# Optimization experiments

Measured on AMD Instinct MI355X. Metric: run time of the kernel, lower is better.

## Reference

```python
import jax, jax.numpy as jnp
import numpy as np

B, T_IN, T_OUT = 256, 256, 32
E, H, Y, V = 512, 1024, 1024, 32000


def gru_cell(x, h, Wih, Whh, bih, bhh):
    # torch GRU gate order: r, z, n
    gi = x @ Wih.T + bih
    gh = h @ Whh.T + bhh
    ir, iz, inn = jnp.split(gi, 3, axis=-1)
    hr, hz, hn = jnp.split(gh, 3, axis=-1)
    r = jax.nn.sigmoid(ir + hr)
    z = jax.nn.sigmoid(iz + hz)
    n = jnp.tanh(inn + r * hn)
    return (1.0 - z) * n + z * h


def setup_inputs() -> dict:
    key = jax.random.key(0)
    ks = jax.random.split(key, 32)
    s = 0.05
    p = lambda k, shape: (jax.random.normal(k, shape, jnp.float32) * s)
    inp = {
        'x': jax.random.randint(ks[0], (B, T_IN), 0, V),
        'y': (jax.random.uniform(ks[1], (B, T_OUT, Y)) < 0.01).astype(jnp.float32),
        'emb': p(ks[2], (V, E)),
        # encoder layer 0 (input E) and layer 1 (input H)
        'enc_Wih0': p(ks[3], (3 * H, E)), 'enc_Whh0': p(ks[4], (3 * H, H)),
        'enc_bih0': p(ks[5], (3 * H,)), 'enc_bhh0': p(ks[6], (3 * H,)),
        'enc_Wih1': p(ks[7], (3 * H, H)), 'enc_Whh1': p(ks[8], (3 * H, H)),
        'enc_bih1': p(ks[9], (3 * H,)), 'enc_bhh1': p(ks[10], (3 * H,)),
        # decoder layer 0 (input Y) and layer 1 (input H)
        'dec_Wih0': p(ks[11], (3 * H, Y)), 'dec_Whh0': p(ks[12], (3 * H, H)),
        'dec_bih0': p(ks[13], (3 * H,)), 'dec_bhh0': p(ks[14], (3 * H,)),
        'dec_Wih1': p(ks[15], (3 * H, H)), 'dec_Whh1': p(ks[16], (3 * H, H)),
        'dec_bih1': p(ks[17], (3 * H,)), 'dec_bhh1': p(ks[18], (3 * H,)),
        # mapping: Linear(2H -> Y) followed by log-softmax
        'map_W': p(ks[19], (Y, 2 * H)), 'map_b': p(ks[20], (Y,)),
    }
    return inp


def reference(x, y, emb,
              enc_Wih0, enc_Whh0, enc_bih0, enc_bhh0,
              enc_Wih1, enc_Whh1, enc_bih1, enc_bhh1,
              dec_Wih0, dec_Whh0, dec_bih0, dec_bhh0,
              dec_Wih1, dec_Whh1, dec_bih1, dec_bhh1,
              map_W, map_b):
    batch = x.shape[0]
    h_dim = enc_Whh0.shape[1]

    # ---- encoder: 2-layer GRU over seq_in, h0 = 0 ----
    seq = emb[x].transpose(1, 0, 2)  # [T_in, B, E]
    finals = []
    for prm in ((enc_Wih0, enc_Whh0, enc_bih0, enc_bhh0),
                (enc_Wih1, enc_Whh1, enc_bih1, enc_bhh1)):
        def step(h, xt, prm=prm):
            hn = gru_cell(xt, h, *prm)
            return hn, hn
        hT, seq = jax.lax.scan(step, jnp.zeros((batch, h_dim), seq.dtype), seq)
        finals.append(hT)
    enc_out = seq.transpose(1, 0, 2)  # [B, T_in, H]

    # ---- decoder: teacher-forced, one step at a time ----
    y_shift = jnp.concatenate([jnp.zeros((batch, 1, y.shape[2]), y.dtype), y[:, :-1]], axis=1)
    ys_in = y_shift.transpose(1, 0, 2)  # [T_out, B, Y]
    ys_t = y.transpose(1, 0, 2)         # [T_out, B, Y]
    dec0 = (dec_Wih0, dec_Whh0, dec_bih0, dec_bhh0)
    dec1 = (dec_Wih1, dec_Whh1, dec_bih1, dec_bhh1)

    def dec_step(carry, inp):
        h1, h2 = carry
        y_in, y_t = inp
        h1 = gru_cell(y_in, h1, *dec0)
        h2 = gru_cell(h1, h2, *dec1)           # dec_out == top-layer hidden
        scores = jnp.einsum('bsh,bh->bs', enc_out, h2)
        alpha = jax.nn.softmax(scores, axis=-1)          # over encoder positions
        attn = jnp.einsum('bsh,bs->bh', enc_out, alpha)  # [B, H]
        logits = jnp.concatenate([attn, h2], axis=1) @ map_W.T + map_b
        logp = jax.nn.log_softmax(logits, axis=-1)
        loss_t = -(logp * y_t).sum()
        return (h1, h2), loss_t

    _, losses = jax.lax.scan(dec_step, (finals[0], finals[1]), (ys_in, ys_t))
    return losses.sum() / y.sum()
```

## Files before the change

### kernel.cpp

```cpp
#include <hip/hip_runtime.h>
#include <hip/hip_bf16.h>
#include <math.h>

#define BATCH 256
#define T_IN 256
#define T_OUT 32
#define E_DIM 512
#define H_DIM 1024
#define Y_DIM 1024
#define G_DIM 3072

typedef __attribute__((ext_vector_type(8))) __bf16 bf16x8;
typedef __attribute__((ext_vector_type(4))) float f32x4;
typedef __attribute__((ext_vector_type(4))) unsigned int u32x4;

__device__ __forceinline__ unsigned short f2bf_raw(float x) {
    unsigned int u = __builtin_bit_cast(unsigned int, x);
    u += 0x7FFFu + ((u >> 16) & 1u);
    return (unsigned short)(u >> 16);
}
__device__ __forceinline__ float bf2f(short s) {
    unsigned int u = ((unsigned int)(unsigned short)s) << 16;
    return __builtin_bit_cast(float, u);
}
__device__ __forceinline__ f32x4 mfma16(bf16x8 a, bf16x8 b, f32x4 c) {
    return __builtin_amdgcn_mfma_f32_16x16x32_bf16(a, b, c, 0, 0, 0);
}
__device__ __forceinline__ bf16x8 ldsb8(const short* p) {
    return __builtin_bit_cast(bf16x8, *(const u32x4*)p);
}

__global__ __launch_bounds__(256) void f32_to_bf16(
    const float* __restrict__ src, short* __restrict__ dst, int n4)
{
    for (int i = blockIdx.x * 256 + threadIdx.x; i < n4; i += gridDim.x * 256) {
        float4 f = *(const float4*)(src + 4 * (size_t)i);
        short4 o;
        o.x = (short)f2bf_raw(f.x);
        o.y = (short)f2bf_raw(f.y);
        o.z = (short)f2bf_raw(f.z);
        o.w = (short)f2bf_raw(f.w);
        *(short4*)(dst + 4 * (size_t)i) = o;
    }
}

struct CellArgs {
    const float* Af; const short* Ab; const int* gat; int gs; int lda; int Kx;
    const short* Wih; const short* Whh;
    const float* bih; const float* bhh;
    const short* hbf;
    const float* hf;
    float* houtf; short* houtbf; short* copy;
    int active;
};

__global__ __launch_bounds__(256) void cell_kernel(CellArgs cA, CellArgs cB)
{
    const CellArgs a = blockIdx.z ? cB : cA;
    if (!a.active) return;

    __shared__ __align__(16) short As[2 * 1280];
    __shared__ __align__(16) short Ws[6 * 2560];

    const int tid = threadIdx.x;
    const int bm = blockIdx.x * 32;
    const int bn = blockIdx.y * 64;

    const int sr = (tid >> 2) & 31;
    const int ss = tid >> 7;
    const int wr = tid >> 2;
    const int ch = (tid & 3) * 8;

    const float* axf = nullptr;
    const short* axb = nullptr;
    if (a.Af) {
        int ridx = a.gat ? a.gat[(size_t)(bm + sr) * a.gs] : (bm + sr);
        axf = a.Af + (size_t)ridx * a.lda + ch;
    } else if (a.Ab) {
        axb = a.Ab + (size_t)(bm + sr) * a.lda + ch;
    }
    const short* ahb = a.hbf + (size_t)(bm + sr) * H_DIM + ch;

    const short* wsrc[6];
    #pragma unroll
    for (int g = 0; g < 3; ++g) {
        wsrc[g]     = a.Wih + (size_t)(g * H_DIM + bn + wr) * a.Kx + ch;
        wsrc[g + 3] = a.Whh + (size_t)(g * H_DIM + bn + wr) * H_DIM + ch;
    }
    short* adst  = &As[ss * 1280 + sr * 40 + ch];
    short* wdst0 = &Ws[wr * 40 + ch];

    const int lane = tid & 63;
    const int w = tid >> 6;
    const int lr = lane & 15;
    const int ko = (lane >> 4) * 8;
    const short* pax0 = &As[lr * 40 + ko];
    const short* pax1 = &As[(16 + lr) * 40 + ko];
    const short* pah0 = &As[1280 + lr * 40 + ko];
    const short* pah1 = &As[1280 + (16 + lr) * 40 + ko];
    const int wc = (w * 16 + lr) * 40 + ko;

    f32x4 accI[3][2] = {{{0.f,0.f,0.f,0.f}}};
    f32x4 accH[3][2] = {{{0.f,0.f,0.f,0.f}}};

    const int Kx = a.Kx;
    for (int k0 = 0; k0 < H_DIM; k0 += 32) {
        const bool xact = (k0 < Kx);
        u32x4 av = {0u, 0u, 0u, 0u};
        if (ss) {
            av = *(const u32x4*)(ahb + k0);
        } else if (xact) {
            if (axb) {
                av = *(const u32x4*)(axb + k0);
            } else if (axf) {
                float4 f0 = *(const float4*)(axf + k0);
                float4 f1 = *(const float4*)(axf + k0 + 4);
                av.x = ((unsigned)f2bf_raw(f0.y) << 16) | f2bf_raw(f0.x);
                av.y = ((unsigned)f2bf_raw(f0.w) << 16) | f2bf_raw(f0.z);
                av.z = ((unsigned)f2bf_raw(f1.y) << 16) | f2bf_raw(f1.x);
                av.w = ((unsigned)f2bf_raw(f1.w) << 16) | f2bf_raw(f1.z);
            }
        }
        if (ss || xact) *(u32x4*)adst = av;
        #pragma unroll
        for (int i = 0; i < 6; ++i) {
            if (i >= 3 || xact)
                *(u32x4*)(wdst0 + i * 2560) = *(const u32x4*)(wsrc[i] + k0);
        }
        __syncthreads();
        bf16x8 ah0 = ldsb8(pah0), ah1 = ldsb8(pah1);
        #pragma unroll
        for (int g = 0; g < 3; ++g) {
            bf16x8 wh = ldsb8(&Ws[(g + 3) * 2560 + wc]);
            accH[g][0] = mfma16(ah0, wh, accH[g][0]);
            accH[g][1] = mfma16(ah1, wh, accH[g][1]);
        }
        if (xact) {
            bf16x8 ax0 = ldsb8(pax0), ax1 = ldsb8(pax1);
            #pragma unroll
            for (int g = 0; g < 3; ++g) {
                bf16x8 wi = ldsb8(&Ws[g * 2560 + wc]);
                accI[g][0] = mfma16(ax0, wi, accI[g][0]);
                accI[g][1] = mfma16(ax1, wi, accI[g][1]);
            }
        }
        __syncthreads();
    }

    const int j = bn + w * 16 + lr;
    const float bi0 = a.bih[j], bi1 = a.bih[H_DIM + j], bi2 = a.bih[2 * H_DIM + j];
    const float bh0 = a.bhh[j], bh1 = a.bhh[H_DIM + j], bh2 = a.bhh[2 * H_DIM + j];
    #pragma unroll
    for (int rh = 0; rh < 2; ++rh) {
        #pragma unroll
        for (int q = 0; q < 4; ++q) {
            int row = bm + rh * 16 + (lane >> 4) * 4 + q;
            float ir = accI[0][rh][q] + bi0, hr = accH[0][rh][q] + bh0;
            float iz = accI[1][rh][q] + bi1, hz = accH[1][rh][q] + bh1;
            float in_ = accI[2][rh][q] + bi2, hn = accH[2][rh][q] + bh2;
            float r = 1.f / (1.f + expf(-(ir + hr)));
            float z = 1.f / (1.f + expf(-(iz + hz)));
            float n = tanhf(in_ + r * hn);
            size_t oi = (size_t)row * H_DIM + j;
            float hv = a.hf[oi];
            float o = (1.f - z) * n + z * hv;
            a.houtf[oi] = o;
            short ob = (short)f2bf_raw(o);
            a.houtbf[oi] = ob;
            if (a.copy) a.copy[oi] = ob;
        }
    }
}

__global__ __launch_bounds__(256) void score_gemm(
    const short* __restrict__ h2all, const short* __restrict__ enc,
    float* __restrict__ S)
{
    const int st = blockIdx.x;
    const int b = blockIdx.y;
    __shared__ __align__(16) short Hs[32 * 40];
    __shared__ __align__(16) short Es[64 * 40];
    const int tid = threadIdx.x;
    const int ch = (tid & 3) * 8;
    const int hrow = (tid >> 2) & 31;
    const int erow = tid >> 2;
    const short* hsrc = h2all + ((size_t)hrow * BATCH + b) * H_DIM + ch;
    const short* esrc = enc + ((size_t)(st * 64 + erow) * BATCH + b) * H_DIM + ch;
    short* hdst = &Hs[hrow * 40 + ch];
    short* edst = &Es[erow * 40 + ch];

    const int lane = tid & 63, w = tid >> 6;
    const int lr = lane & 15, ko = (lane >> 4) * 8;
    f32x4 acc0 = {0.f, 0.f, 0.f, 0.f}, acc1 = acc0;
    for (int k0 = 0; k0 < H_DIM; k0 += 32) {
        if (tid < 128) *(u32x4*)hdst = *(const u32x4*)(hsrc + k0);
        *(u32x4*)edst = *(const u32x4*)(esrc + k0);
        __syncthreads();
        bf16x8 e = ldsb8(&Es[(w * 16 + lr) * 40 + ko]);
        bf16x8 h0v = ldsb8(&Hs[lr * 40 + ko]);
        bf16x8 h1v = ldsb8(&Hs[(16 + lr) * 40 + ko]);
        acc0 = mfma16(h0v, e, acc0);
        acc1 = mfma16(h1v, e, acc1);
        __syncthreads();
    }
    int s = st * 64 + w * 16 + lr;
    #pragma unroll
    for (int q = 0; q < 4; ++q) {
        int t0 = (lane >> 4) * 4 + q;
        S[(size_t)b * 8192 + (size_t)t0 * 256 + s] = acc0[q];
        S[(size_t)b * 8192 + (size_t)(t0 + 16) * 256 + s] = acc1[q];
    }
}

__global__ __launch_bounds__(256) void softmax_all(float* __restrict__ S)
{
    size_t base = (size_t)blockIdx.x * 256;
    int t = threadIdx.x;
    float v = S[base + t];
    int lane = t & 63, w = t >> 6;
    float m = v;
    for (int off = 32; off; off >>= 1) m = fmaxf(m, __shfl_down(m, off));
    __shared__ float r1[4];
    if (!lane) r1[w] = m;
    __syncthreads();
    m = fmaxf(fmaxf(r1[0], r1[1]), fmaxf(r1[2], r1[3]));
    float ex = expf(v - m);
    float s = ex;
    for (int off = 32; off; off >>= 1) s += __shfl_down(s, off);
    __shared__ float r2[4];
    if (!lane) r2[w] = s;
    __syncthreads();
    s = r2[0] + r2[1] + r2[2] + r2[3];
    S[base + t] = ex / s;
}

__global__ __launch_bounds__(256) void attn_apply_all(
    const short* __restrict__ enc, const float* __restrict__ S,
    short* __restrict__ attn_bf)
{
    const int tc = blockIdx.x, b = blockIdx.y;
    __shared__ float al[8][256];
    const int tid = threadIdx.x;
    #pragma unroll
    for (int ti = 0; ti < 8; ++ti)
        al[ti][tid] = S[(size_t)b * 8192 + (size_t)(tc * 8 + ti) * 256 + tid];
    __syncthreads();
    float acc[8][4] = {};
    const short* eb = enc + (size_t)b * H_DIM + tid;
    for (int s = 0; s < 256; ++s) {
        const short* er = eb + (size_t)s * (BATCH * H_DIM);
        float e0 = bf2f(er[0]), e1 = bf2f(er[256]);
        float e2 = bf2f(er[512]), e3 = bf2f(er[768]);
        #pragma unroll
        for (int ti = 0; ti < 8; ++ti) {
            float av = al[ti][s];
            acc[ti][0] += av * e0; acc[ti][1] += av * e1;
            acc[ti][2] += av * e2; acc[ti][3] += av * e3;
        }
    }
    #pragma unroll
    for (int ti = 0; ti < 8; ++ti) {
        size_t m = (size_t)(tc * 8 + ti) * 256 + b;
        #pragma unroll
        for (int i = 0; i < 4; ++i)
            attn_bf[m * H_DIM + tid + i * 256] = (short)f2bf_raw(acc[ti][i]);
    }
}

__global__ __launch_bounds__(256) void map_gemm(
    const short* __restrict__ A1, const short* __restrict__ A2,
    const short* __restrict__ Wm, const float* __restrict__ bias,
    float* __restrict__ C)
{
    const int bm = blockIdx.x * 64, bn = blockIdx.y * 64;
    __shared__ __align__(16) short S1[64 * 40], S2[64 * 40], T1[64 * 40], T2[64 * 40];
    const int tid = threadIdx.x;
    const int r = tid >> 2, ch = (tid & 3) * 8;
    const short* a1 = A1 + (size_t)(bm + r) * 1024 + ch;
    const short* a2 = A2 + (size_t)(bm + r) * 1024 + ch;
    const short* w1 = Wm + (size_t)(bn + r) * 2048 + ch;
    const short* w2 = w1 + 1024;
    const int lane = tid & 63, w = tid >> 6;
    const int wm = (w >> 1) * 32, wn = (w & 1) * 32;
    const int lr = lane & 15, ko = (lane >> 4) * 8;
    f32x4 acc[2][2] = {{{0.f,0.f,0.f,0.f}}};
    for (int k0 = 0; k0 < 1024; k0 += 32) {
        *(u32x4*)&S1[r * 40 + ch] = *(const u32x4*)(a1 + k0);
        *(u32x4*)&S2[r * 40 + ch] = *(const u32x4*)(a2 + k0);
        *(u32x4*)&T1[r * 40 + ch] = *(const u32x4*)(w1 + k0);
        *(u32x4*)&T2[r * 40 + ch] = *(const u32x4*)(w2 + k0);
        __syncthreads();
        bf16x8 x1[2], x2[2], y1[2], y2[2];
        #pragma unroll
        for (int i = 0; i < 2; ++i) {
            x1[i] = ldsb8(&S1[(wm + i * 16 + lr) * 40 + ko]);
            x2[i] = ldsb8(&S2[(wm + i * 16 + lr) * 40 + ko]);
            y1[i] = ldsb8(&T1[(wn + i * 16 + lr) * 40 + ko]);
            y2[i] = ldsb8(&T2[(wn + i * 16 + lr) * 40 + ko]);
        }
        #pragma unroll
        for (int i = 0; i < 2; ++i) {
            #pragma unroll
            for (int jq = 0; jq < 2; ++jq) {
                acc[i][jq] = mfma16(x1[i], y1[jq], acc[i][jq]);
                acc[i][jq] = mfma16(x2[i], y2[jq], acc[i][jq]);
            }
        }
        __syncthreads();
    }
    #pragma unroll
    for (int i = 0; i < 2; ++i) {
        #pragma unroll
        for (int jq = 0; jq < 2; ++jq) {
            int col = bn + wn + jq * 16 + lr;
            float bv = bias[col];
            #pragma unroll
            for (int q = 0; q < 4; ++q) {
                int row = bm + wm + i * 16 + (lane >> 4) * 4 + q;
                C[(size_t)row * 1024 + col] = acc[i][jq][q] + bv;
            }
        }
    }
}

__global__ __launch_bounds__(256) void loss_all(
    const float* __restrict__ logits, const float* __restrict__ y,
    float* __restrict__ loss_acc)
{
    int m = blockIdx.x, t = threadIdx.x;
    int tt = m >> 8, b = m & 255;
    const float* lrow = logits + (size_t)m * Y_DIM;
    float l[4];
    #pragma unroll
    for (int i = 0; i < 4; ++i) l[i] = lrow[t + i * 256];
    float mx = fmaxf(fmaxf(l[0], l[1]), fmaxf(l[2], l[3]));
    int lane = t & 63, w = t >> 6;
    for (int off = 32; off; off >>= 1) mx = fmaxf(mx, __shfl_down(mx, off));
    __shared__ float sm[4];
    if (!lane) sm[w] = mx;
    __syncthreads();
    mx = fmaxf(fmaxf(sm[0], sm[1]), fmaxf(sm[2], sm[3]));
    float es = 0.f;
    #pragma unroll
    for (int i = 0; i < 4; ++i) es += expf(l[i] - mx);
    for (int off = 32; off; off >>= 1) es += __shfl_down(es, off);
    __shared__ float ss[4];
    if (!lane) ss[w] = es;
    __syncthreads();
    float sum = ss[0] + ss[1] + ss[2] + ss[3];
    float logZ = mx + logf(sum);
    const float* yrow = y + ((size_t)b * T_OUT + tt) * Y_DIM;
    float part = 0.f;
    #pragma unroll
    for (int i = 0; i < 4; ++i) part += yrow[t + i * 256] * (logZ - l[i]);
    for (int off = 32; off; off >>= 1) part += __shfl_down(part, off);
    __shared__ float sp[4];
    if (!lane) sp[w] = part;
    __syncthreads();
    if (t == 0) atomicAdd(loss_acc, sp[0] + sp[1] + sp[2] + sp[3]);
}

__global__ __launch_bounds__(256) void ysum_kernel(
    const float* __restrict__ y, float* __restrict__ ysum, int n)
{
    float s = 0.f;
    for (int i = blockIdx.x * 256 + threadIdx.x; i < n; i += gridDim.x * 256)
        s += y[i];
    int lane = threadIdx.x & 63, w = threadIdx.x >> 6;
    for (int off = 32; off; off >>= 1) s += __shfl_down(s, off);
    __shared__ float sw[4];
    if (!lane) sw[w] = s;
    __syncthreads();
    if (!threadIdx.x) atomicAdd(ysum, sw[0] + sw[1] + sw[2] + sw[3]);
}

__global__ __launch_bounds__(256) void init_kernel(
    float* __restrict__ h0, float* __restrict__ h1,
    short* __restrict__ h0b, short* __restrict__ h1b,
    float* __restrict__ loss, float* __restrict__ ysum)
{
    int i = blockIdx.x * 256 + threadIdx.x;
    h0[i] = 0.f; h1[i] = 0.f; h0b[i] = 0; h1b[i] = 0;
    if (i == 0) { *loss = 0.f; *ysum = 0.f; }
}

__global__ void final_kernel(const float* __restrict__ loss,
                             const float* __restrict__ ysum,
                             float* __restrict__ out)
{
    if (threadIdx.x == 0) out[0] = loss[0] / ysum[0];
}

extern "C" void kernel_launch(void* const* d_in, const int* in_sizes, int n_in,
                              void* d_out, int out_size, void* d_ws, size_t ws_size,
                              hipStream_t stream)
{
    const int*   x     = (const int*)d_in[0];
    const float* y     = (const float*)d_in[1];
    const float* emb   = (const float*)d_in[2];
    const float* eWih0 = (const float*)d_in[3];
    const float* eWhh0 = (const float*)d_in[4];
    const float* ebih0 = (const float*)d_in[5];
    const float* ebhh0 = (const float*)d_in[6];
    const float* eWih1 = (const float*)d_in[7];
    const float* eWhh1 = (const float*)d_in[8];
    const float* ebih1 = (const float*)d_in[9];
    const float* ebhh1 = (const float*)d_in[10];
    const float* dWih0 = (const float*)d_in[11];
    const float* dWhh0 = (const float*)d_in[12];
    const float* dbih0 = (const float*)d_in[13];
    const float* dbhh0 = (const float*)d_in[14];
    const float* dWih1 = (const float*)d_in[15];
    const float* dWhh1 = (const float*)d_in[16];
    const float* dbih1 = (const float*)d_in[17];
    const float* dbhh1 = (const float*)d_in[18];
    const float* mapW  = (const float*)d_in[19];
    const float* mapb  = (const float*)d_in[20];
    float* out = (float*)d_out;

    char* p = (char*)d_ws;
    auto take = [&](size_t n) { char* q = p; p += (n + 255) & ~(size_t)255; return q; };
    short* enc_bf = (short*)take((size_t)T_IN * BATCH * H_DIM * 2);
    char* wslab = p;
    short* eWih0b = (short*)take((size_t)G_DIM * E_DIM * 2);
    short* eWhh0b = (short*)take((size_t)G_DIM * H_DIM * 2);
    short* eWih1b = (short*)take((size_t)G_DIM * H_DIM * 2);
    short* eWhh1b = (short*)take((size_t)G_DIM * H_DIM * 2);
    short* dWih0b = (short*)take((size_t)G_DIM * Y_DIM * 2);
    short* dWhh0b = (short*)take((size_t)G_DIM * H_DIM * 2);
    short* dWih1b = (short*)take((size_t)G_DIM * H_DIM * 2);
    short* dWhh1b = (short*)take((size_t)G_DIM * H_DIM * 2);
    short* mapWb  = (short*)take((size_t)Y_DIM * 2 * H_DIM * 2);
    float* h0f[2]; float* h1f[2]; short* h0b[2]; short* h1b[2];
    for (int i = 0; i < 2; ++i) {
        h0f[i] = (float*)take((size_t)BATCH * H_DIM * 4);
        h1f[i] = (float*)take((size_t)BATCH * H_DIM * 4);
        h0b[i] = (short*)take((size_t)BATCH * H_DIM * 2);
        h1b[i] = (short*)take((size_t)BATCH * H_DIM * 2);
    }
    short* h2all = (short*)take((size_t)T_OUT * BATCH * H_DIM * 2);
    float* loss_acc = (float*)take(256);
    float* ysum = loss_acc + 1;
    float* logits  = (float*)enc_bf;
    short* attn_bf = (short*)wslab;
    float* S       = (float*)(wslab + (size_t)20 * 1024 * 1024);

    dim3 blk(256);

    f32_to_bf16<<<dim3(512), blk, 0, stream>>>(eWih0, eWih0b, G_DIM * E_DIM / 4);
    f32_to_bf16<<<dim3(512), blk, 0, stream>>>(eWhh0, eWhh0b, G_DIM * H_DIM / 4);
    f32_to_bf16<<<dim3(512), blk, 0, stream>>>(eWih1, eWih1b, G_DIM * H_DIM / 4);
    f32_to_bf16<<<dim3(512), blk, 0, stream>>>(eWhh1, eWhh1b, G_DIM * H_DIM / 4);
    f32_to_bf16<<<dim3(512), blk, 0, stream>>>(dWih0, dWih0b, G_DIM * Y_DIM / 4);
    f32_to_bf16<<<dim3(512), blk, 0, stream>>>(dWhh0, dWhh0b, G_DIM * H_DIM / 4);
    f32_to_bf16<<<dim3(512), blk, 0, stream>>>(dWih1, dWih1b, G_DIM * H_DIM / 4);
    f32_to_bf16<<<dim3(512), blk, 0, stream>>>(dWhh1, dWhh1b, G_DIM * H_DIM / 4);
    f32_to_bf16<<<dim3(512), blk, 0, stream>>>(mapW, mapWb, Y_DIM * 2 * H_DIM / 4);

    init_kernel<<<dim3(BATCH * H_DIM / 256), blk, 0, stream>>>(
        h0f[0], h1f[0], h0b[0], h1b[0], loss_acc, ysum);
    ysum_kernel<<<dim3(2048), blk, 0, stream>>>(y, ysum, BATCH * T_OUT * Y_DIM);

    dim3 gCell(8, 16, 2);

    for (int k = 0; k <= T_IN; ++k) {
        CellArgs A = {}, B = {};
        A.active = (k < T_IN);
        if (A.active) {
            A.Af = emb; A.gat = x + k; A.gs = T_IN; A.lda = E_DIM; A.Kx = E_DIM;
            A.Wih = eWih0b; A.Whh = eWhh0b; A.bih = ebih0; A.bhh = ebhh0;
            A.hbf = h0b[k & 1]; A.hf = h0f[k & 1];
            A.houtf = h0f[(k + 1) & 1]; A.houtbf = h0b[(k + 1) & 1];
        }
        B.active = (k >= 1);
        if (B.active) {
            B.Ab = h0b[k & 1]; B.lda = H_DIM; B.Kx = H_DIM;
            B.Wih = eWih1b; B.Whh = eWhh1b; B.bih = ebih1; B.bhh = ebhh1;
            B.hbf = h1b[(k - 1) & 1]; B.hf = h1f[(k - 1) & 1];
            B.houtf = h1f[k & 1]; B.houtbf = h1b[k & 1];
            B.copy = enc_bf + (size_t)(k - 1) * BATCH * H_DIM;
        }
        cell_kernel<<<gCell, blk, 0, stream>>>(A, B);
    }

    for (int k = 0; k <= T_OUT; ++k) {
        CellArgs A = {}, B = {};
        A.active = (k < T_OUT);
        if (A.active) {
            A.Af = (k == 0) ? nullptr : (y + (size_t)(k - 1) * Y_DIM);
            A.lda = T_OUT * Y_DIM; A.Kx = Y_DIM;
            A.Wih = dWih0b; A.Whh = dWhh0b; A.bih = dbih0; A.bhh = dbhh0;
            A.hbf = h0b[k & 1]; A.hf = h0f[k & 1];
            A.houtf = h0f[(k + 1) & 1]; A.houtbf = h0b[(k + 1) & 1];
        }
        B.active = (k >= 1);
        if (B.active) {
            B.Ab = h0b[k & 1]; B.lda = H_DIM; B.Kx = H_DIM;
            B.Wih = dWih1b; B.Whh = dWhh1b; B.bih = dbih1; B.bhh = dbhh1;
            B.hbf = h1b[(k - 1) & 1]; B.hf = h1f[(k - 1) & 1];
            B.houtf = h1f[k & 1]; B.houtbf = h1b[k & 1];
            B.copy = h2all + (size_t)(k - 1) * BATCH * H_DIM;
        }
        cell_kernel<<<gCell, blk, 0, stream>>>(A, B);
    }

    score_gemm<<<dim3(4, 256), blk, 0, stream>>>(h2all, enc_bf, S);
    softmax_all<<<dim3(8192), blk, 0, stream>>>(S);
    attn_apply_all<<<dim3(4, 256), blk, 0, stream>>>(enc_bf, S, attn_bf);
    map_gemm<<<dim3(128, 16), blk, 0, stream>>>(attn_bf, h2all, mapWb, mapb, logits);
    loss_all<<<dim3(8192), blk, 0, stream>>>(logits, y, loss_acc);

    final_kernel<<<dim3(1), dim3(64), 0, stream>>>(loss_acc, ysum, out);
}
```

Before: 15.23 ms.

## Rewrite GRU cell kernel with double-buffered weights and register-direct activation fragments

Replaces the GRU cell kernel with a version that retiles each block to 64 rows by 32 columns and uses a flat 256-block grid whose index swizzle groups blocks sharing weight columns. Weight tiles are double-buffered in shared memory and the next tile is prefetched into registers, so only one barrier is needed per k-step. Activation (x and h) fragments are loaded straight from global memory into MFMA operand registers instead of passing through LDS. The aim is to hide global latency and cut barriers and LDS traffic in the latency-bound recurrent steps. The cost is more register pressure and uncoalesced per-lane activation loads.

New measurement: 19.35 ms. 1.27x slower.

```diff
diff --git a/kernel.cpp b/kernel.cpp
--- a/kernel.cpp
+++ b/kernel.cpp
@@ -28,6 +28,23 @@
 }
 __device__ __forceinline__ bf16x8 ldsb8(const short* p) {
     return __builtin_bit_cast(bf16x8, *(const u32x4*)p);
+}
+__device__ __forceinline__ bf16x8 zero_bf8() {
+    u32x4 z = {0u, 0u, 0u, 0u};
+    return __builtin_bit_cast(bf16x8, z);
+}
+__device__ __forceinline__ bf16x8 load_bf8(const short* p) {
+    return __builtin_bit_cast(bf16x8, *(const u32x4*)p);
+}
+__device__ __forceinline__ bf16x8 load_f32_as_bf8(const float* p) {
+    float4 f0 = *(const float4*)p;
+    float4 f1 = *(const float4*)(p + 4);
+    u32x4 v;
+    v.x = ((unsigned)f2bf_raw(f0.y) << 16) | f2bf_raw(f0.x);
+    v.y = ((unsigned)f2bf_raw(f0.w) << 16) | f2bf_raw(f0.z);
+    v.z = ((unsigned)f2bf_raw(f1.y) << 16) | f2bf_raw(f1.x);
+    v.w = ((unsigned)f2bf_raw(f1.w) << 16) | f2bf_raw(f1.z);
+    return __builtin_bit_cast(bf16x8, v);
 }
 
 __global__ __launch_bounds__(256) void f32_to_bf16(
@@ -54,114 +71,144 @@
     int active;
 };
 
-__global__ __launch_bounds__(256) void cell_kernel(CellArgs cA, CellArgs cB)
-{
-    const CellArgs a = blockIdx.z ? cB : cA;
+__global__ __launch_bounds__(256) void cell2(CellArgs cA, CellArgs cB)
+{
+    const int id = blockIdx.x;
+    const CellArgs a = (id >= 128) ? cB : cA;
     if (!a.active) return;
-
-    __shared__ __align__(16) short As[2 * 1280];
-    __shared__ __align__(16) short Ws[6 * 2560];
+    const int cid = id & 127;
+    const int nt = (cid & 7) * 4 + (cid >> 5);
+    const int mt = (cid >> 3) & 3;
+    const int bm = mt * 64;
+    const int bn = nt * 32;
+
+    __shared__ __align__(16) short Ws[2][192 * 40];
 
     const int tid = threadIdx.x;
-    const int bm = blockIdx.x * 32;
-    const int bn = blockIdx.y * 64;
-
-    const int sr = (tid >> 2) & 31;
-    const int ss = tid >> 7;
-    const int wr = tid >> 2;
-    const int ch = (tid & 3) * 8;
-
-    const float* axf = nullptr;
-    const short* axb = nullptr;
-    if (a.Af) {
-        int ridx = a.gat ? a.gat[(size_t)(bm + sr) * a.gs] : (bm + sr);
-        axf = a.Af + (size_t)ridx * a.lda + ch;
-    } else if (a.Ab) {
-        axb = a.Ab + (size_t)(bm + sr) * a.lda + ch;
-    }
-    const short* ahb = a.hbf + (size_t)(bm + sr) * H_DIM + ch;
-
-    const short* wsrc[6];
-    #pragma unroll
-    for (int g = 0; g < 3; ++g) {
-        wsrc[g]     = a.Wih + (size_t)(g * H_DIM + bn + wr) * a.Kx + ch;
-        wsrc[g + 3] = a.Whh + (size_t)(g * H_DIM + bn + wr) * H_DIM + ch;
-    }
-    short* adst  = &As[ss * 1280 + sr * 40 + ch];
-    short* wdst0 = &Ws[wr * 40 + ch];
-
     const int lane = tid & 63;
     const int w = tid >> 6;
+    const int wm = w & 1;
+    const int wn = w >> 1;
     const int lr = lane & 15;
-    const int ko = (lane >> 4) * 8;
-    const short* pax0 = &As[lr * 40 + ko];
-    const short* pax1 = &As[(16 + lr) * 40 + ko];
-    const short* pah0 = &As[1280 + lr * 40 + ko];
-    const short* pah1 = &As[1280 + (16 + lr) * 40 + ko];
-    const int wc = (w * 16 + lr) * 40 + ko;
-
-    f32x4 accI[3][2] = {{{0.f,0.f,0.f,0.f}}};
-    f32x4 accH[3][2] = {{{0.f,0.f,0.f,0.f}}};
-
+    const int lk = lane >> 4;
     const int Kx = a.Kx;
+
+    const short* wsrc[3];
+    int woff[3];
+    int wlim[3];
+    #pragma unroll
+    for (int j = 0; j < 3; ++j) {
+        int lin = j * 256 + tid;
+        int r = lin >> 2, c = lin & 3;
+        bool ih = (r < 96);
+        int rr = ih ? r : r - 96;
+        int g = rr >> 5;
+        int col = bn + (rr & 31);
+        const short* base = ih ? a.Wih : a.Whh;
+        int K = ih ? Kx : H_DIM;
+        wsrc[j] = base + (size_t)(g * H_DIM + col) * K + c * 8;
+        woff[j] = r * 40 + c * 8;
+        wlim[j] = ih ? Kx : H_DIM;
+    }
+
+    const short* ah0p; const short* ah1p;
+    const short* axb0 = nullptr; const short* axb1 = nullptr;
+    const float* axf0 = nullptr; const float* axf1 = nullptr;
+    {
+        int r0 = bm + wm * 32 + lr;
+        int r1 = r0 + 16;
+        ah0p = a.hbf + (size_t)r0 * H_DIM + lk * 8;
+        ah1p = a.hbf + (size_t)r1 * H_DIM + lk * 8;
+        if (Kx > 0) {
+            if (a.Ab) {
+                axb0 = a.Ab + (size_t)r0 * a.lda + lk * 8;
+                axb1 = a.Ab + (size_t)r1 * a.lda + lk * 8;
+            } else {
+                int i0 = a.gat ? a.gat[(size_t)r0 * a.gs] : r0;
+                int i1 = a.gat ? a.gat[(size_t)r1 * a.gs] : r1;
+                axf0 = a.Af + (size_t)i0 * a.lda + lk * 8;
+                axf1 = a.Af + (size_t)i1 * a.lda + lk * 8;
+            }
+        }
+    }
+
+    f32x4 zf = {0.f, 0.f, 0.f, 0.f};
+    f32x4 accI[3][2] = {{zf, zf}, {zf, zf}, {zf, zf}};
+    f32x4 accH[3][2] = {{zf, zf}, {zf, zf}, {zf, zf}};
+
+    #pragma unroll
+    for (int j = 0; j < 3; ++j)
+        if (wlim[j] > 0) *(u32x4*)&Ws[0][woff[j]] = *(const u32x4*)(wsrc[j]);
+    bf16x8 aH0 = load_bf8(ah0p), aH1 = load_bf8(ah1p);
+    bf16x8 aX0 = zero_bf8(), aX1 = zero_bf8();
+    if (Kx > 0) {
+        if (axb0) { aX0 = load_bf8(axb0); aX1 = load_bf8(axb1); }
+        else      { aX0 = load_f32_as_bf8(axf0); aX1 = load_f32_as_bf8(axf1); }
+    }
+    __syncthreads();
+
+    int cur = 0;
     for (int k0 = 0; k0 < H_DIM; k0 += 32) {
-        const bool xact = (k0 < Kx);
-        u32x4 av = {0u, 0u, 0u, 0u};
-        if (ss) {
-            av = *(const u32x4*)(ahb + k0);
-        } else if (xact) {
-            if (axb) {
-                av = *(const u32x4*)(axb + k0);
-            } else if (axf) {
-                float4 f0 = *(const float4*)(axf + k0);
-                float4 f1 = *(const float4*)(axf + k0 + 4);
-                av.x = ((unsigned)f2bf_raw(f0.y) << 16) | f2bf_raw(f0.x);
-                av.y = ((unsigned)f2bf_raw(f0.w) << 16) | f2bf_raw(f0.z);
-                av.z = ((unsigned)f2bf_raw(f1.y) << 16) | f2bf_raw(f1.x);
-                av.w = ((unsigned)f2bf_raw(f1.w) << 16) | f2bf_raw(f1.z);
+        const int kn = k0 + 32;
+        const bool more = kn < H_DIM;
+
+        u32x4 wreg[3]; bool wact[3];
+        #pragma unroll
+        for (int j = 0; j < 3; ++j) {
+            wact[j] = more && (kn < wlim[j]);
+            if (wact[j]) wreg[j] = *(const u32x4*)(wsrc[j] + kn);
+        }
+        bf16x8 aH0n = zero_bf8(), aH1n = zero_bf8();
+        bf16x8 aX0n = zero_bf8(), aX1n = zero_bf8();
+        if (more) {
+            aH0n = load_bf8(ah0p + kn); aH1n = load_bf8(ah1p + kn);
+            if (kn < Kx) {
+                if (axb0) { aX0n = load_bf8(axb0 + kn); aX1n = load_bf8(axb1 + kn); }
+                else      { aX0n = load_f32_as_bf8(axf0 + kn); aX1n = load_f32_as_bf8(axf1 + kn); }
             }
         }
-        if (ss || xact) *(u32x4*)adst = av;
-        #pragma unroll
-        for (int i = 0; i < 6; ++i) {
-            if (i >= 3 || xact)
-                *(u32x4*)(wdst0 + i * 2560) = *(const u32x4*)(wsrc[i] + k0);
-        }
-        __syncthreads();
-        bf16x8 ah0 = ldsb8(pah0), ah1 = ldsb8(pah1);
+
+        const short* wb = Ws[cur];
         #pragma unroll
         for (int g = 0; g < 3; ++g) {
-            bf16x8 wh = ldsb8(&Ws[(g + 3) * 2560 + wc]);
-            accH[g][0] = mfma16(ah0, wh, accH[g][0]);
-            accH[g][1] = mfma16(ah1, wh, accH[g][1]);
-        }
-        if (xact) {
-            bf16x8 ax0 = ldsb8(pax0), ax1 = ldsb8(pax1);
+            bf16x8 wh = ldsb8(&wb[(96 + g * 32 + wn * 16 + lr) * 40 + lk * 8]);
+            accH[g][0] = mfma16(aH0, wh, accH[g][0]);
+            accH[g][1] = mfma16(aH1, wh, accH[g][1]);
+        }
+        if (k0 < Kx) {
             #pragma unroll
             for (int g = 0; g < 3; ++g) {
-                bf16x8 wi = ldsb8(&Ws[g * 2560 + wc]);
-                accI[g][0] = mfma16(ax0, wi, accI[g][0]);
-                accI[g][1] = mfma16(ax1, wi, accI[g][1]);
+                bf16x8 wi = ldsb8(&wb[(g * 32 + wn * 16 + lr) * 40 + lk * 8]);
+                accI[g][0] = mfma16(aX0, wi, accI[g][0]);
+                accI[g][1] = mfma16(aX1, wi, accI[g][1]);
             }
         }
+
+        short* wo = Ws[cur ^ 1];
+        #pragma unroll
+        for (int j = 0; j < 3; ++j)
+            if (wact[j]) *(u32x4*)&wo[woff[j]] = wreg[j];
         __syncthreads();
-    }
-
-    const int j = bn + w * 16 + lr;
-    const float bi0 = a.bih[j], bi1 = a.bih[H_DIM + j], bi2 = a.bih[2 * H_DIM + j];
-    const float bh0 = a.bhh[j], bh1 = a.bhh[H_DIM + j], bh2 = a.bhh[2 * H_DIM + j];
-    #pragma unroll
-    for (int rh = 0; rh < 2; ++rh) {
+
+        aH0 = aH0n; aH1 = aH1n; aX0 = aX0n; aX1 = aX1n;
+        cur ^= 1;
+    }
+
+    const int col = bn + wn * 16 + lr;
+    const float bi0 = a.bih[col], bi1 = a.bih[H_DIM + col], bi2 = a.bih[2 * H_DIM + col];
+    const float bh0 = a.bhh[col], bh1 = a.bhh[H_DIM + col], bh2 = a.bhh[2 * H_DIM + col];
+    #pragma unroll
+    for (int mf = 0; mf < 2; ++mf) {
         #pragma unroll
         for (int q = 0; q < 4; ++q) {
-            int row = bm + rh * 16 + (lane >> 4) * 4 + q;
-            float ir = accI[0][rh][q] + bi0, hr = accH[0][rh][q] + bh0;
-            float iz = accI[1][rh][q] + bi1, hz = accH[1][rh][q] + bh1;
-            float in_ = accI[2][rh][q] + bi2, hn = accH[2][rh][q] + bh2;
+            int row = bm + wm * 32 + mf * 16 + (lane >> 4) * 4 + q;
+            float ir = accI[0][mf][q] + bi0, hr = accH[0][mf][q] + bh0;
+            float iz = accI[1][mf][q] + bi1, hz = accH[1][mf][q] + bh1;
+            float in_ = accI[2][mf][q] + bi2, hn = accH[2][mf][q] + bh2;
             float r = 1.f / (1.f + expf(-(ir + hr)));
             float z = 1.f / (1.f + expf(-(iz + hz)));
             float n = tanhf(in_ + r * hn);
-            size_t oi = (size_t)row * H_DIM + j;
+            size_t oi = (size_t)row * H_DIM + col;
             float hv = a.hf[oi];
             float o = (1.f - z) * n + z * hv;
             a.houtf[oi] = o;
@@ -461,8 +508,6 @@
         h0f[0], h1f[0], h0b[0], h1b[0], loss_acc, ysum);
     ysum_kernel<<<dim3(2048), blk, 0, stream>>>(y, ysum, BATCH * T_OUT * Y_DIM);
 
-    dim3 gCell(8, 16, 2);
-
     for (int k = 0; k <= T_IN; ++k) {
         CellArgs A = {}, B = {};
         A.active = (k < T_IN);
@@ -480,15 +525,19 @@
             B.houtf = h1f[k & 1]; B.houtbf = h1b[k & 1];
             B.copy = enc_bf + (size_t)(k - 1) * BATCH * H_DIM;
         }
-        cell_kernel<<<gCell, blk, 0, stream>>>(A, B);
+        cell2<<<dim3(256), blk, 0, stream>>>(A, B);
     }
 
     for (int k = 0; k <= T_OUT; ++k) {
         CellArgs A = {}, B = {};
         A.active = (k < T_OUT);
         if (A.active) {
-            A.Af = (k == 0) ? nullptr : (y + (size_t)(k - 1) * Y_DIM);
-            A.lda = T_OUT * Y_DIM; A.Kx = Y_DIM;
+            if (k == 0) {
+                A.Kx = 0;
+            } else {
+                A.Af = y + (size_t)(k - 1) * Y_DIM;
+                A.lda = T_OUT * Y_DIM; A.Kx = Y_DIM;
+            }
             A.Wih = dWih0b; A.Whh = dWhh0b; A.bih = dbih0; A.bhh = dbhh0;
             A.hbf = h0b[k & 1]; A.hf = h0f[k & 1];
             A.houtf = h0f[(k + 1) & 1]; A.houtbf = h0b[(k + 1) & 1];
@@ -501,7 +550,7 @@
             B.houtf = h1f[k & 1]; B.houtbf = h1b[k & 1];
             B.copy = h2all + (size_t)(k - 1) * BATCH * H_DIM;
         }
-        cell_kernel<<<gCell, blk, 0, stream>>>(A, B);
+        cell2<<<dim3(256), blk, 0, stream>>>(A, B);
     }
 
     score_gemm<<<dim3(4, 256), blk, 0, stream>>>(h2all, enc_bf, S);
```

## Shrink GRU cell tiles to 32x32 for more blocks and swizzled grid

Applied to the files above, without the earlier changes.

Replaces the GRU cell kernel with a 32x32 output tile per block, so 512 blocks (256 per layer) are launched instead of 256. Each wave now owns one 16x16 sub-tile, and the LDS row stride drops to 34 shorts. Block ids are remapped so neighbouring blocks share weight columns, and launch bounds request two blocks per CU. The aim is to fill more CUs on the latency-bound recurrent steps, at the cost of reloading each weight tile from global memory twice as often. The decoder's first step sets Kx=0 so the input-side GEMM is skipped entirely rather than computed on zeros.

After: 22.44 ms. 47.3% more time.

```diff
diff --git a/kernel.cpp b/kernel.cpp
--- a/kernel.cpp
+++ b/kernel.cpp
@@ -9,6 +9,7 @@
 #define H_DIM 1024
 #define Y_DIM 1024
 #define G_DIM 3072
+#define RS 34
 
 typedef __attribute__((ext_vector_type(8))) __bf16 bf16x8;
 typedef __attribute__((ext_vector_type(4))) float f32x4;
@@ -28,6 +29,16 @@
 }
 __device__ __forceinline__ bf16x8 ldsb8(const short* p) {
     return __builtin_bit_cast(bf16x8, *(const u32x4*)p);
+}
+__device__ __forceinline__ u32x4 conv_f32x8(const float* p) {
+    float4 f0 = *(const float4*)p;
+    float4 f1 = *(const float4*)(p + 4);
+    u32x4 v;
+    v.x = ((unsigned)f2bf_raw(f0.y) << 16) | f2bf_raw(f0.x);
+    v.y = ((unsigned)f2bf_raw(f0.w) << 16) | f2bf_raw(f0.z);
+    v.z = ((unsigned)f2bf_raw(f1.y) << 16) | f2bf_raw(f1.x);
+    v.w = ((unsigned)f2bf_raw(f1.w) << 16) | f2bf_raw(f1.z);
+    return v;
 }
 
 __global__ __launch_bounds__(256) void f32_to_bf16(
@@ -54,121 +65,115 @@
     int active;
 };
 
-__global__ __launch_bounds__(256) void cell_kernel(CellArgs cA, CellArgs cB)
-{
-    const CellArgs a = blockIdx.z ? cB : cA;
+__global__ __launch_bounds__(256, 2) void cell3(CellArgs cA, CellArgs cB)
+{
+    const int id = blockIdx.x;
+    const CellArgs a = (id >= 256) ? cB : cA;
     if (!a.active) return;
-
-    __shared__ __align__(16) short As[2 * 1280];
-    __shared__ __align__(16) short Ws[6 * 2560];
+    const int cid = id & 255;
+    const int nt = (cid & 7) * 4 + ((cid >> 3) & 3);
+    const int mt = cid >> 5;
+    const int bm = mt * 32, bn = nt * 32;
+
+    __shared__ __align__(16) short As[2 * 32 * RS];
+    __shared__ __align__(16) short Ws[192 * RS];
 
     const int tid = threadIdx.x;
-    const int bm = blockIdx.x * 32;
-    const int bn = blockIdx.y * 64;
-
-    const int sr = (tid >> 2) & 31;
-    const int ss = tid >> 7;
-    const int wr = tid >> 2;
-    const int ch = (tid & 3) * 8;
-
-    const float* axf = nullptr;
-    const short* axb = nullptr;
-    if (a.Af) {
-        int ridx = a.gat ? a.gat[(size_t)(bm + sr) * a.gs] : (bm + sr);
-        axf = a.Af + (size_t)ridx * a.lda + ch;
-    } else if (a.Ab) {
-        axb = a.Ab + (size_t)(bm + sr) * a.lda + ch;
-    }
-    const short* ahb = a.hbf + (size_t)(bm + sr) * H_DIM + ch;
-
-    const short* wsrc[6];
-    #pragma unroll
-    for (int g = 0; g < 3; ++g) {
-        wsrc[g]     = a.Wih + (size_t)(g * H_DIM + bn + wr) * a.Kx + ch;
-        wsrc[g + 3] = a.Whh + (size_t)(g * H_DIM + bn + wr) * H_DIM + ch;
-    }
-    short* adst  = &As[ss * 1280 + sr * 40 + ch];
-    short* wdst0 = &Ws[wr * 40 + ch];
-
     const int lane = tid & 63;
     const int w = tid >> 6;
-    const int lr = lane & 15;
-    const int ko = (lane >> 4) * 8;
-    const short* pax0 = &As[lr * 40 + ko];
-    const short* pax1 = &As[(16 + lr) * 40 + ko];
-    const short* pah0 = &As[1280 + lr * 40 + ko];
-    const short* pah1 = &As[1280 + (16 + lr) * 40 + ko];
-    const int wc = (w * 16 + lr) * 40 + ko;
-
-    f32x4 accI[3][2] = {{{0.f,0.f,0.f,0.f}}};
-    f32x4 accH[3][2] = {{{0.f,0.f,0.f,0.f}}};
-
+    const int wm = w & 1, wn = w >> 1;
+    const int lr = lane & 15, lk = lane >> 4;
     const int Kx = a.Kx;
+
+    const int ss = tid >> 7;
+    const int sr = (tid >> 2) & 31;
+    const int ch = (tid & 3) * 8;
+    const float* axf = nullptr; const short* axb = nullptr;
+    if (ss == 0 && Kx > 0) {
+        if (a.Ab) {
+            axb = a.Ab + (size_t)(bm + sr) * a.lda + ch;
+        } else {
+            int ridx = a.gat ? a.gat[(size_t)(bm + sr) * a.gs] : (bm + sr);
+            axf = a.Af + (size_t)ridx * a.lda + ch;
+        }
+    }
+    const short* ahs = a.hbf + (size_t)(bm + sr) * H_DIM + ch;
+    short* adst = &As[ss * (32 * RS) + sr * RS + ch];
+
+    const short* wsrc[3]; int woff[3]; int wlim[3];
+    #pragma unroll
+    for (int j = 0; j < 3; ++j) {
+        int lin = j * 256 + tid;
+        int r = lin >> 2, c = lin & 3;
+        bool ih = (r < 96);
+        int rr = ih ? r : r - 96;
+        int g = rr >> 5;
+        int col = bn + (rr & 31);
+        int K = ih ? Kx : H_DIM;
+        wsrc[j] = (ih ? a.Wih : a.Whh) + (size_t)(g * H_DIM + col) * K + c * 8;
+        woff[j] = r * RS + c * 8;
+        wlim[j] = K;
+    }
+
+    const short* pax = &As[(wm * 16 + lr) * RS + lk * 8];
+    const short* pah = &As[32 * RS + (wm * 16 + lr) * RS + lk * 8];
+
+    f32x4 zf = {0.f, 0.f, 0.f, 0.f};
+    f32x4 accI[3] = {zf, zf, zf};
+    f32x4 accH[3] = {zf, zf, zf};
+
     for (int k0 = 0; k0 < H_DIM; k0 += 32) {
-        const bool xact = (k0 < Kx);
-        u32x4 av = {0u, 0u, 0u, 0u};
-        if (ss) {
-            av = *(const u32x4*)(ahb + k0);
-        } else if (xact) {
-            if (axb) {
-                av = *(const u32x4*)(axb + k0);
-            } else if (axf) {
-                float4 f0 = *(const float4*)(axf + k0);
-                float4 f1 = *(const float4*)(axf + k0 + 4);
-                av.x = ((unsigned)f2bf_raw(f0.y) << 16) | f2bf_raw(f0.x);
-                av.y = ((unsigned)f2bf_raw(f0.w) << 16) | f2bf_raw(f0.z);
-                av.z = ((unsigned)f2bf_raw(f1.y) << 16) | f2bf_raw(f1.x);
-                av.w = ((unsigned)f2bf_raw(f1.w) << 16) | f2bf_raw(f1.z);
+        if (ss == 0) {
+            if (k0 < Kx) {
+                u32x4 av;
+                if (axb) av = *(const u32x4*)(axb + k0);
+                else     av = conv_f32x8(axf + k0);
+                *(u32x4*)adst = av;
             }
-        }
-        if (ss || xact) *(u32x4*)adst = av;
-        #pragma unroll
-        for (int i = 0; i < 6; ++i) {
-            if (i >= 3 || xact)
-                *(u32x4*)(wdst0 + i * 2560) = *(const u32x4*)(wsrc[i] + k0);
-        }
+        } else {
+            *(u32x4*)adst = *(const u32x4*)(ahs + k0);
+        }
+        #pragma unroll
+        for (int j = 0; j < 3; ++j)
+            if (k0 < wlim[j]) *(u32x4*)&Ws[woff[j]] = *(const u32x4*)(wsrc[j] + k0);
         __syncthreads();
-        bf16x8 ah0 = ldsb8(pah0), ah1 = ldsb8(pah1);
+
+        bf16x8 aH = ldsb8(pah);
         #pragma unroll
         for (int g = 0; g < 3; ++g) {
-            bf16x8 wh = ldsb8(&Ws[(g + 3) * 2560 + wc]);
-            accH[g][0] = mfma16(ah0, wh, accH[g][0]);
-            accH[g][1] = mfma16(ah1, wh, accH[g][1]);
-        }
-        if (xact) {
-            bf16x8 ax0 = ldsb8(pax0), ax1 = ldsb8(pax1);
+            bf16x8 wh = ldsb8(&Ws[(96 + g * 32 + wn * 16 + lr) * RS + lk * 8]);
+            accH[g] = mfma16(aH, wh, accH[g]);
+        }
+        if (k0 < Kx) {
+            bf16x8 aX = ldsb8(pax);
             #pragma unroll
             for (int g = 0; g < 3; ++g) {
-                bf16x8 wi = ldsb8(&Ws[g * 2560 + wc]);
-                accI[g][0] = mfma16(ax0, wi, accI[g][0]);
-                accI[g][1] = mfma16(ax1, wi, accI[g][1]);
+                bf16x8 wi = ldsb8(&Ws[(g * 32 + wn * 16 + lr) * RS + lk * 8]);
+                accI[g] = mfma16(aX, wi, accI[g]);
             }
         }
         __syncthreads();
     }
 
-    const int j = bn + w * 16 + lr;
-    const float bi0 = a.bih[j], bi1 = a.bih[H_DIM + j], bi2 = a.bih[2 * H_DIM + j];
-    const float bh0 = a.bhh[j], bh1 = a.bhh[H_DIM + j], bh2 = a.bhh[2 * H_DIM + j];
-    #pragma unroll
-    for (int rh = 0; rh < 2; ++rh) {
-        #pragma unroll
-        for (int q = 0; q < 4; ++q) {
-            int row = bm + rh * 16 + (lane >> 4) * 4 + q;
-            float ir = accI[0][rh][q] + bi0, hr = accH[0][rh][q] + bh0;
-            float iz = accI[1][rh][q] + bi1, hz = accH[1][rh][q] + bh1;
-            float in_ = accI[2][rh][q] + bi2, hn = accH[2][rh][q] + bh2;
-            float r = 1.f / (1.f + expf(-(ir + hr)));
-            float z = 1.f / (1.f + expf(-(iz + hz)));
-            float n = tanhf(in_ + r * hn);
-            size_t oi = (size_t)row * H_DIM + j;
-            float hv = a.hf[oi];
-            float o = (1.f - z) * n + z * hv;
-            a.houtf[oi] = o;
-            short ob = (short)f2bf_raw(o);
-            a.houtbf[oi] = ob;
-            if (a.copy) a.copy[oi] = ob;
-        }
+    const int colj = bn + wn * 16 + lr;
+    const float bi0 = a.bih[colj], bi1 = a.bih[H_DIM + colj], bi2 = a.bih[2 * H_DIM + colj];
+    const float bh0 = a.bhh[colj], bh1 = a.bhh[H_DIM + colj], bh2 = a.bhh[2 * H_DIM + colj];
+    #pragma unroll
+    for (int q = 0; q < 4; ++q) {
+        int row = bm + wm * 16 + lk * 4 + q;
+        float ir = accI[0][q] + bi0, hr = accH[0][q] + bh0;
+        float iz = accI[1][q] + bi1, hz = accH[1][q] + bh1;
+        float in_ = accI[2][q] + bi2, hn = accH[2][q] + bh2;
+        float r = 1.f / (1.f + expf(-(ir + hr)));
+        float z = 1.f / (1.f + expf(-(iz + hz)));
+        float n = tanhf(in_ + r * hn);
+        size_t oi = (size_t)row * H_DIM + colj;
+        float hv = a.hf[oi];
+        float o = (1.f - z) * n + z * hv;
+        a.houtf[oi] = o;
+        short ob = (short)f2bf_raw(o);
+        a.houtbf[oi] = ob;
+        if (a.copy) a.copy[oi] = ob;
     }
 }
 
@@ -461,8 +466,6 @@
         h0f[0], h1f[0], h0b[0], h1b[0], loss_acc, ysum);
     ysum_kernel<<<dim3(2048), blk, 0, stream>>>(y, ysum, BATCH * T_OUT * Y_DIM);
 
-    dim3 gCell(8, 16, 2);
-
     for (int k = 0; k <= T_IN; ++k) {
         CellArgs A = {}, B = {};
         A.active = (k < T_IN);
@@ -480,15 +483,19 @@
             B.houtf = h1f[k & 1]; B.houtbf = h1b[k & 1];
             B.copy = enc_bf + (size_t)(k - 1) * BATCH * H_DIM;
         }
-        cell_kernel<<<gCell, blk, 0, stream>>>(A, B);
+        cell3<<<dim3(512), blk, 0, stream>>>(A, B);
     }
 
     for (int k = 0; k <= T_OUT; ++k) {
         CellArgs A = {}, B = {};
         A.active = (k < T_OUT);
         if (A.active) {
-            A.Af = (k == 0) ? nullptr : (y + (size_t)(k - 1) * Y_DIM);
-            A.lda = T_OUT * Y_DIM; A.Kx = Y_DIM;
+            if (k == 0) {
+                A.Kx = 0;
+            } else {
+                A.Af = y + (size_t)(k - 1) * Y_DIM;
+                A.lda = T_OUT * Y_DIM; A.Kx = Y_DIM;
+            }
             A.Wih = dWih0b; A.Whh = dWhh0b; A.bih = dbih0; A.bhh = dbhh0;
             A.hbf = h0b[k & 1]; A.hf = h0f[k & 1];
             A.houtf = h0f[(k + 1) & 1]; A.houtbf = h0b[(k + 1) & 1];
@@ -501,7 +508,7 @@
             B.houtf = h1f[k & 1]; B.houtbf = h1b[k & 1];
             B.copy = h2all + (size_t)(k - 1) * BATCH * H_DIM;
         }
-        cell_kernel<<<gCell, blk, 0, stream>>>(A, B);
+        cell3<<<dim3(512), blk, 0, stream>>>(A, B);
     }
 
     score_gemm<<<dim3(4, 256), blk, 0, stream>>>(h2all, enc_bf, S);
```
